# Performance work log

Hardware: AMD Instinct MI355X
Metric: run time of the kernel (lower is better)

Reference implementation:

```python
import jax, jax.numpy as jnp
import numpy as np

NV, NG, D, K, NB = 4096, 2048, 64, 128, 4
C_IN, C_OUT, E = 128, 8, 32768
SIGMA = 2.5  # rbf sigma used in the non-mp path


def _gcn_conv(x, src, dst, w, b, n):
    # PyG GCNConv (edge_weight=None, self loops already appended to src/dst)
    deg = jax.ops.segment_sum(jnp.ones(src.shape, x.dtype), dst, num_segments=n)
    dinv = jnp.where(deg > 0, 1.0 / jnp.sqrt(deg), 0.0)
    norm = dinv[src] * dinv[dst]
    h = x @ w
    return jax.ops.segment_sum(h[src] * norm[:, None], dst, num_segments=n) + b


def _diff_block(x, mass, evals, evecs, gradX, gradY, t, a_re, a_im, w0, b0, w1, b1, w2, b2):
    # learned-time spectral diffusion
    x_spec = evecs.T @ (x * mass[:, None])                      # [K, D]
    coef = jnp.exp(-evals[:, None] * jnp.clip(t, 1e-8)[None, :])  # [K, D]
    x_diff = evecs @ (coef * x_spec)                            # [NV, D]
    # spatial gradient features: complex grad, learned rotation, tanh of inner product
    gX = gradX @ x_diff                                         # real part  [NV, D]
    gY = gradY @ x_diff                                         # imag part  [NV, D]
    b_re = gX @ a_re - gY @ a_im
    b_im = gY @ a_re + gX @ a_im
    gfeat = jnp.tanh(gX * b_re + gY * b_im)
    f = jnp.concatenate([x, x_diff, gfeat], axis=-1)            # [NV, 3D]
    h = jax.nn.relu(f @ w0 + b0)
    h = jax.nn.relu(h @ w1 + b1)
    return h @ w2 + b2 + x                                      # residual skip


def _forward(surf_x, mass, evals, evecs, gradX, gradY, vertices, graph_x, graph_pos,
             lin1_w, lin1_b, lin2_w, lin2_b, last_w, last_b,
             diff_time, A_re, A_im, mlp_w0, mlp_b0, mlp_w1, mlp_b1, mlp_w2, mlp_b2,
             gcn_w1, gcn_b1, gcn_w2, gcn_b2, edge_index):
    nv, ng = vertices.shape[0], graph_pos.shape[0]
    # dense rbf coupling (torch.no_grad in original -> stop_gradient)
    d2 = (jnp.sum(vertices * vertices, 1)[:, None]
          + jnp.sum(graph_pos * graph_pos, 1)[None, :]
          - 2.0 * (vertices @ graph_pos.T))
    dist = jnp.sqrt(jnp.clip(d2, 0.0))
    rbf = jax.lax.stop_gradient(jnp.exp(-dist / SIGMA))          # [NV, NG]
    diff_x = surf_x @ lin1_w + lin1_b                            # [NV, D]
    gx = graph_x @ lin2_w + lin2_b                               # [NG, D]
    loops = jnp.arange(ng, dtype=edge_index.dtype)
    src = jnp.concatenate([edge_index[0], loops])
    dst = jnp.concatenate([edge_index[1], loops])
    for i in range(NB):
        diff_x = _diff_block(diff_x, mass, evals, evecs, gradX, gradY,
                             diff_time[i], A_re[i], A_im[i],
                             mlp_w0[i], mlp_b0[i], mlp_w1[i], mlp_b1[i], mlp_w2[i], mlp_b2[i])
        gx = rbf.T @ diff_x                                      # surface -> graph
        h = jax.nn.relu(_gcn_conv(gx, src, dst, gcn_w1[i], gcn_b1[i], ng))
        gx = _gcn_conv(h, src, dst, gcn_w2[i], gcn_b2[i], ng)
        diff_x = rbf @ gx                                        # graph -> surface
    return diff_x @ last_w + last_b                              # [NV, C_OUT]


def setup_inputs() -> dict:
    key = jax.random.key(0)
    ks = jax.random.split(key, 24)
    f32 = jnp.float32
    def rn(k, shape, scale=1.0):
        return jax.random.normal(k, shape, f32) * scale
    inp = {
        'surf_x': rn(ks[0], (NV, 5)),
        'mass': jax.random.uniform(ks[1], (NV,), f32, 0.1, 1.0),
        'evals': jnp.sort(jax.random.uniform(ks[2], (K,), f32, 0.0, 50.0)),
        'evecs': rn(ks[3], (NV, K), 1.0 / np.sqrt(NV)),
        'gradX': rn(ks[4], (NV, NV), 1.0 / np.sqrt(NV)),
        'gradY': rn(ks[5], (NV, NV), 1.0 / np.sqrt(NV)),
        'vertices': rn(ks[6], (NV, 3), 5.0),
        'graph_x': rn(ks[7], (NG, C_IN)),
        'graph_pos': rn(ks[8], (NG, 3), 5.0),
        'lin1_w': rn(ks[9], (5, D), 1.0 / np.sqrt(5)),
        'lin1_b': jnp.zeros((D,), f32),
        'lin2_w': rn(ks[10], (C_IN, D), 1.0 / np.sqrt(C_IN)),
        'lin2_b': jnp.zeros((D,), f32),
        'last_w': rn(ks[11], (D, C_OUT), 1.0 / np.sqrt(D)),
        'last_b': jnp.zeros((C_OUT,), f32),
        'diff_time': jax.random.uniform(ks[12], (NB, D), f32, 1e-3, 1.0),
        'A_re': rn(ks[13], (NB, D, D), 1.0 / np.sqrt(D)),
        'A_im': rn(ks[14], (NB, D, D), 1.0 / np.sqrt(D)),
        'mlp_w0': rn(ks[15], (NB, 3 * D, D), 1.0 / np.sqrt(3 * D)),
        'mlp_b0': jnp.zeros((NB, D), f32),
        'mlp_w1': rn(ks[16], (NB, D, D), 1.0 / np.sqrt(D)),
        'mlp_b1': jnp.zeros((NB, D), f32),
        'mlp_w2': rn(ks[17], (NB, D, D), 1.0 / np.sqrt(D)),
        'mlp_b2': jnp.zeros((NB, D), f32),
        'gcn_w1': rn(ks[18], (NB, D, D), 1.0 / np.sqrt(D)),
        'gcn_b1': jnp.zeros((NB, D), f32),
        'gcn_w2': rn(ks[19], (NB, D, D), 1.0 / np.sqrt(D)),
        'gcn_b2': jnp.zeros((NB, D), f32),
        'edge_index': jax.random.randint(ks[20], (2, E), 0, NG, dtype=jnp.int32),
    }
    return inp


def reference(surf_x, mass, evals, evecs, gradX, gradY, vertices, graph_x, graph_pos,
              lin1_w, lin1_b, lin2_w, lin2_b, last_w, last_b,
              diff_time, A_re, A_im, mlp_w0, mlp_b0, mlp_w1, mlp_b1, mlp_w2, mlp_b2,
              gcn_w1, gcn_b1, gcn_w2, gcn_b2, edge_index):
    return _forward(surf_x, mass, evals, evecs, gradX, gradY, vertices, graph_x, graph_pos,
                    lin1_w, lin1_b, lin2_w, lin2_b, last_w, last_b,
                    diff_time, A_re, A_im, mlp_w0, mlp_b0, mlp_w1, mlp_b1, mlp_w2, mlp_b2,
                    gcn_w1, gcn_b1, gcn_w2, gcn_b2, edge_index)
```

## Files before the change

### kernel.cpp

```cpp
#include <hip/hip_runtime.h>
#include <hip/hip_bf16.h>

#define NVV 4096
#define NGG 2048
#define DD 64
#define KSP 128
#define NBLK 4
#define NEDGE 32768
#define COUT 8
#define NSLICE_P 8
#define NSLICE_G 16
#define NSLICE_V 8
#define NSLICE_S 32
#define VS 32

typedef __hip_bfloat16 bf16;
using bf16x8 = __attribute__((ext_vector_type(8))) __bf16;
using s16x8  = __attribute__((ext_vector_type(8))) short;
using f32x4  = __attribute__((ext_vector_type(4))) float;

__device__ __forceinline__ float toF(bf16 x){ return __bfloat162float(x); }
__device__ __forceinline__ float ldin(const void* p, size_t i, int f){
  return f ? toF(((const bf16*)p)[i]) : ((const float*)p)[i];
}
__device__ __forceinline__ short f2bf(float x){
  __bf16 b = (__bf16)x;
  return __builtin_bit_cast(short, b);
}
__device__ __forceinline__ float bf2f(short s){
  return (float)__builtin_bit_cast(__bf16, s);
}
__device__ __forceinline__ bf16x8 ld8(const short* p){
  return __builtin_bit_cast(bf16x8, *(const s16x8*)p);
}
__device__ __forceinline__ void gl16(const short* g, short* l){
  __builtin_amdgcn_global_load_lds((__attribute__((address_space(1))) void*)(g),
                                   (__attribute__((address_space(3))) void*)(l),
                                   16, 0, 0);
}

__global__ void k_probe(const void* __restrict__ mass, int* __restrict__ flag){
  int t = threadIdx.x;
  float v = toF(((const bf16*)mass)[t]);
  bool ok = (v >= 0.05f) && (v <= 1.05f);
  unsigned long long m = __ballot(ok);
  if (t == 0) flag[0] = (m == ~0ull) ? 1 : 0;
}

__global__ void k_csr_zero(int* c){ int g = blockIdx.x*256+threadIdx.x; if (g<NGG) c[g]=0; }
__global__ void k_csr_cnt(const int* __restrict__ ei, int* __restrict__ c){
  int e = blockIdx.x*256+threadIdx.x; if (e<NEDGE) atomicAdd(&c[ei[NEDGE+e]], 1);
}
__global__ void k_csr_scan(const int* __restrict__ cnt, int* __restrict__ off,
                           int* __restrict__ cursor, float* __restrict__ dinv){
  __shared__ int ws[256];
  int t = threadIdx.x;
  int base = t*8;
  int local[8]; int s = 0;
  #pragma unroll
  for (int i=0;i<8;i++){ local[i]=s; s += cnt[base+i]; }
  ws[t] = s;
  __syncthreads();
  for (int o=1;o<256;o<<=1){
    int v = (t>=o) ? ws[t-o] : 0;
    __syncthreads();
    ws[t] += v;
    __syncthreads();
  }
  int pre = (t==0) ? 0 : ws[t-1];
  #pragma unroll
  for (int i=0;i<8;i++){
    int o = pre + local[i];
    off[base+i] = o; cursor[base+i] = o;
    dinv[base+i] = rsqrtf(1.f + (float)cnt[base+i]);
  }
  if (t==255) off[NGG] = pre + s;
}
__global__ void k_csr_fill(const int* __restrict__ ei, int* __restrict__ cursor,
                           int* __restrict__ csrc){
  int e = blockIdx.x*256+threadIdx.x;
  if (e < NEDGE){
    int d = ei[NEDGE+e];
    int p = atomicAdd(&cursor[d], 1);
    csrc[p] = ei[e];
  }
}

__global__ void k_lin1_mx(const void* __restrict__ sx, const void* __restrict__ w,
                          const void* __restrict__ b, const void* __restrict__ mass,
                          float* __restrict__ out, short* __restrict__ btMX,
                          const int* __restrict__ flg){
  const int f = *flg;
  __shared__ short tl[64*68];
  const int t = threadIdx.x;
  const int r = t>>2, c0 = (t&3)*16;
  const size_t v = (size_t)blockIdx.x*64 + r;
  float sxa[5];
  #pragma unroll
  for (int k=0;k<5;k++) sxa[k] = ldin(sx, v*5+k, f);
  const float mv = ldin(mass, v, f);
  float acc[16];
  #pragma unroll
  for (int j=0;j<16;j++){
    float a = ldin(b, c0+j, f);
    #pragma unroll
    for (int k=0;k<5;k++) a += sxa[k]*ldin(w, (size_t)k*DD + c0 + j, f);
    acc[j] = a;
    tl[(size_t)(c0+j)*68 + r] = f2bf(a*mv);
  }
  float* op = out + v*DD + c0;
  ((float4*)op)[0] = *(float4*)&acc[0];
  ((float4*)op)[1] = *(float4*)&acc[4];
  ((float4*)op)[2] = *(float4*)&acc[8];
  ((float4*)op)[3] = *(float4*)&acc[12];
  __syncthreads();
  s16x8 u0, u1;
  #pragma unroll
  for (int j=0;j<8;j++){ u0[j]=tl[(size_t)r*68+c0+j]; u1[j]=tl[(size_t)r*68+c0+8+j]; }
  const int s8 = (r&7)<<3;
  short* dp = btMX + (size_t)blockIdx.x*4096 + (size_t)r*64;
  *(s16x8*)&dp[c0 ^ s8]     = u0;
  *(s16x8*)&dp[(c0+8) ^ s8] = u1;
}

__global__ void k_spec_red(const float* __restrict__ partial, const void* __restrict__ evals,
                           const void* __restrict__ tvec, int boff,
                           short* __restrict__ btA, const int* __restrict__ flg){
  const int f = *flg;
  int idx = blockIdx.x*256 + threadIdx.x;
  int k = idx >> 6, d = idx & 63;
  float sum = 0.f;
  #pragma unroll 8
  for (int s = 0; s < VS; s++) sum += partial[(size_t)s*KSP*DD + idx];
  float t = fmaxf(ldin(tvec, boff + d, f), 1e-8f);
  float val = expf(-ldin(evals, k, f) * t) * sum;
  btA[(size_t)(k>>6)*4096 + (size_t)d*64 + ((k&63) ^ ((d&7)<<3))] = f2bf(val);
}

__global__ void k_cvt_a(const void* __restrict__ src, short* __restrict__ dst,
                        int Kfull, const int* __restrict__ flg){
  const int f = *flg;
  const int t = threadIdx.x;
  const int r = t>>2, c0 = (t&3)*16;
  const size_t row = (size_t)blockIdx.x*64 + r;
  const size_t base = row*(size_t)Kfull + (size_t)blockIdx.y*64 + c0;
  s16x8 v0, v1;
  if (f){
    const short* sp = (const short*)src + base;
    v0 = ((const s16x8*)sp)[0];
    v1 = ((const s16x8*)sp)[1];
  } else {
    const float* sp = (const float*)src + base;
    float tmp[16];
    ((float4*)tmp)[0] = ((const float4*)sp)[0];
    ((float4*)tmp)[1] = ((const float4*)sp)[1];
    ((float4*)tmp)[2] = ((const float4*)sp)[2];
    ((float4*)tmp)[3] = ((const float4*)sp)[3];
    #pragma unroll
    for (int i=0;i<8;i++){ v0[i]=f2bf(tmp[i]); v1[i]=f2bf(tmp[8+i]); }
  }
  const int s8 = (r&7)<<3;
  short* dp = dst + ((size_t)blockIdx.x*(Kfull>>6) + blockIdx.y)*4096 + (size_t)r*64;
  *(s16x8*)&dp[c0 ^ s8]     = v0;
  *(s16x8*)&dp[(c0+8) ^ s8] = v1;
}

__global__ void k_cvt_at(const void* __restrict__ evecs, short* __restrict__ dst,
                         const int* __restrict__ flg){
  const int f = *flg;
  __shared__ short tl[64*68];
  const int t = threadIdx.x;
  const int r = t>>2, c0 = (t&3)*16;
  const int kt = blockIdx.x, s = blockIdx.y;
  const size_t v = (size_t)kt*64 + r;
  #pragma unroll
  for (int j=0;j<16;j++)
    tl[(size_t)(c0+j)*68 + r] = f2bf(ldin(evecs, v*KSP + (size_t)s*64 + c0 + j, f));
  __syncthreads();
  s16x8 u0, u1;
  #pragma unroll
  for (int j=0;j<8;j++){ u0[j]=tl[(size_t)r*68+c0+j]; u1[j]=tl[(size_t)r*68+c0+8+j]; }
  const int s8 = (r&7)<<3;
  short* dp = dst + ((size_t)s*64 + kt)*4096 + (size_t)r*64;
  *(s16x8*)&dp[c0 ^ s8]     = u0;
  *(s16x8*)&dp[(c0+8) ^ s8] = u1;
}

__global__ void k_rbf_pre(const void* __restrict__ P, const void* __restrict__ Q,
                          short* __restrict__ rbfV, short* __restrict__ rbfG,
                          const int* __restrict__ flg){
  const int f = *flg;
  __shared__ short tl[64*68];
  const int t = threadIdx.x;
  const int r = t>>2, c0 = (t&3)*16;
  const int vt = blockIdx.x, gt = blockIdx.y;
  const float px = ldin(P, ((size_t)vt*64+r)*3+0, f);
  const float py = ldin(P, ((size_t)vt*64+r)*3+1, f);
  const float pz = ldin(P, ((size_t)vt*64+r)*3+2, f);
  s16x8 v0, v1;
  #pragma unroll
  for (int j=0;j<16;j++){
    const size_t g = (size_t)gt*64 + c0 + j;
    float dx = px - ldin(Q, g*3+0, f);
    float dy = py - ldin(Q, g*3+1, f);
    float dz = pz - ldin(Q, g*3+2, f);
    short s = f2bf(__expf(-sqrtf(dx*dx+dy*dy+dz*dz)*0.4f));
    if (j<8) v0[j] = s; else v1[j-8] = s;
    tl[(size_t)(c0+j)*68 + r] = s;
  }
  const int s8 = (r&7)<<3;
  short* vp = rbfV + ((size_t)vt*(NGG/64) + gt)*4096 + (size_t)r*64;
  *(s16x8*)&vp[c0 ^ s8]     = v0;
  *(s16x8*)&vp[(c0+8) ^ s8] = v1;
  __syncthreads();
  s16x8 u0, u1;
  #pragma unroll
  for (int j=0;j<8;j++){ u0[j] = tl[(size_t)r*68 + c0 + j]; u1[j] = tl[(size_t)r*68 + c0 + 8 + j]; }
  short* gp = rbfG + ((size_t)gt*(NVV/64) + vt)*4096 + (size_t)r*64;
  *(s16x8*)&gp[c0 ^ s8]     = u0;
  *(s16x8*)&gp[(c0+8) ^ s8] = u1;
}

__global__ void k_cvt_wt(const void* __restrict__ Are, const void* __restrict__ Aim,
                         const void* __restrict__ w0, const void* __restrict__ w1,
                         const void* __restrict__ w2,
                         short* __restrict__ btRe, short* __restrict__ btIm,
                         short* __restrict__ btW0, short* __restrict__ btW1,
                         short* __restrict__ btW2, const int* __restrict__ flg){
  const int f = *flg;
  __shared__ short tl[64*68];
  const int t = threadIdx.x;
  const int r = t>>2, c0 = (t&3)*16;
  const int slot = blockIdx.x, b = blockIdx.y;
  const void* src; size_t soff; short* dst; float scale = 1.f;
  switch(slot){
    case 0: src=Are; soff=(size_t)b*4096; dst=btRe + (size_t)b*2*4096;               break;
    case 1: src=Aim; soff=(size_t)b*4096; dst=btRe + (size_t)b*2*4096 + 4096; scale=-1.f; break;
    case 2: src=Aim; soff=(size_t)b*4096; dst=btIm + (size_t)b*2*4096;               break;
    case 3: src=Are; soff=(size_t)b*4096; dst=btIm + (size_t)b*2*4096 + 4096;        break;
    case 4: case 5: case 6:
      src=w0; soff=(size_t)b*3*4096 + (size_t)(slot-4)*4096;
      dst=btW0 + (size_t)b*3*4096 + (size_t)(slot-4)*4096;                           break;
    case 7: src=w1; soff=(size_t)b*4096; dst=btW1 + (size_t)b*4096;                  break;
    default: src=w2; soff=(size_t)b*4096; dst=btW2 + (size_t)b*4096;                 break;
  }
  #pragma unroll
  for (int j=0;j<16;j++)
    tl[(size_t)(c0+j)*68 + r] = f2bf(scale * ldin(src, soff + (size_t)r*64 + c0 + j, f));
  __syncthreads();
  s16x8 u0, u1;
  #pragma unroll
  for (int j=0;j<8;j++){ u0[j]=tl[(size_t)r*68+c0+j]; u1[j]=tl[(size_t)r*68+c0+8+j]; }
  const int s8 = (r&7)<<3;
  short* dp = dst + (size_t)r*64;
  *(s16x8*)&dp[c0 ^ s8]     = u0;
  *(s16x8*)&dp[(c0+8) ^ s8] = u1;
}

template<int TWO>
__global__ void k_gemm_pre(const short* __restrict__ A0, const short* __restrict__ A1,
                           const short* __restrict__ Bt, float* __restrict__ C,
                           int M, int ktt, int tps, int yoff, short* __restrict__ btOut){
  constexpr int NBUF = TWO ? 3 : 2;
  __shared__ __align__(16) short sm[2*NBUF*4096];
  const int t = threadIdx.x;
  const int w = t>>6, lane = t&63;
  const int fr = lane&15, fq = lane>>4;
  const int strip = blockIdx.x, sl = blockIdx.y;
  const size_t abase = ((size_t)strip*ktt + (size_t)sl*tps)*4096;
  const short* gA0 = A0 + abase;
  const short* gA1 = TWO ? (A1 + abase) : A0;
  const short* gB  = Bt + (size_t)sl*tps*4096;
  const int to = t*8;

  auto stage = [&](int p, int kt){
    short* l = &sm[p*NBUF*4096];
    const size_t ko = (size_t)kt*4096;
    gl16(gA0 + ko + to,        l + (w<<9));
    gl16(gA0 + ko + 2048 + to, l + 2048 + (w<<9));
    if (TWO){
      gl16(gA1 + ko + to,        l + 4096 + (w<<9));
      gl16(gA1 + ko + 2048 + to, l + 6144 + (w<<9));
    }
    short* lb = l + (TWO ? 8192 : 4096);
    gl16(gB + ko + to,        lb + (w<<9));
    gl16(gB + ko + 2048 + to, lb + 2048 + (w<<9));
  };

  f32x4 acc0[4] = {{0,0,0,0},{0,0,0,0},{0,0,0,0},{0,0,0,0}};
  f32x4 acc1[4] = {{0,0,0,0},{0,0,0,0},{0,0,0,0},{0,0,0,0}};

  stage(0, 0);
  int cur = 0;
  const int arow = w*16 + fr;
  const int ax0 = arow*64;
  const int asw = (arow&7)<<3;
  for (int kt=0; kt<tps; ++kt){
    if (kt+1 < tps){
      stage(cur^1, kt+1);
      if constexpr (TWO) asm volatile("s_waitcnt vmcnt(6)" ::: "memory");
      else               asm volatile("s_waitcnt vmcnt(4)" ::: "memory");
    } else {
      asm volatile("s_waitcnt vmcnt(0)" ::: "memory");
    }
    __builtin_amdgcn_s_barrier();
    asm volatile("" ::: "memory");
    const short* As  = &sm[cur*NBUF*4096];
    const short* A1s = As + 4096;
    const short* Bs  = As + (TWO ? 8192 : 4096);
    #pragma unroll
    for (int ks=0; ks<2; ks++){
      const int kx = ks*32 + fq*8;
      bf16x8 a0 = ld8(&As[ax0 + (kx ^ asw)]);
      bf16x8 a1 = TWO ? ld8(&A1s[ax0 + (kx ^ asw)]) : a0;
      #pragma unroll
      for (int nc=0;nc<4;nc++){
        const int brow = nc*16 + fr;
        bf16x8 b = ld8(&Bs[brow*64 + (kx ^ ((brow&7)<<3))]);
        acc0[nc] = __builtin_amdgcn_mfma_f32_16x16x32_bf16(a0, b, acc0[nc], 0, 0, 0);
        if constexpr (TWO)
          acc1[nc] = __builtin_amdgcn_mfma_f32_16x16x32_bf16(a1, b, acc1[nc], 0, 0, 0);
      }
    }
    asm volatile("" ::: "memory");
    __builtin_amdgcn_s_barrier();
    cur ^= 1;
  }
  float* C0 = C + (size_t)sl*M*DD;
  const int row0 = strip*64 + w*16 + fq*4;
  #pragma unroll
  for (int nc=0;nc<4;nc++)
    #pragma unroll
    for (int r=0;r<4;r++)
      C0[(size_t)(row0+r)*DD + nc*16 + fr] = acc0[nc][r];
  if constexpr (TWO){
    float* C1 = C + (size_t)yoff + (size_t)sl*M*DD;
    #pragma unroll
    for (int nc=0;nc<4;nc++)
      #pragma unroll
      for (int r=0;r<4;r++)
        C1[(size_t)(row0+r)*DD + nc*16 + fr] = acc1[nc][r];
  }
  if (btOut){
    #pragma unroll
    for (int nc=0;nc<4;nc++)
      #pragma unroll
      for (int r=0;r<4;r++){
        int k = row0 + r, n = nc*16 + fr;
        btOut[(size_t)(k>>6)*4096 + (size_t)n*64 + ((k&63) ^ ((n&7)<<3))] = f2bf(acc0[nc][r]);
      }
  }
}

__global__ void k_fold_at(const float* __restrict__ part, short* __restrict__ dX,
                          short* __restrict__ dY, int s){
  const int t = threadIdx.x;
  const int r = t>>2, c0 = (t&3)*16;
  const int strip = blockIdx.x;
  float ax[16], ay[16];
  #pragma unroll
  for (int j=0;j<16;j++){ ax[j]=0.f; ay[j]=0.f; }
  const float* pb = part + ((size_t)strip*64 + r)*DD + c0;
  for (int sl=0; sl<NSLICE_P; sl++){
    const float* px = pb + (size_t)sl*NVV*DD;
    const float* py = pb + (size_t)(sl+NSLICE_P)*NVV*DD;
    #pragma unroll
    for (int q=0;q<4;q++){
      float4 a = ((const float4*)px)[q];
      float4 b = ((const float4*)py)[q];
      ax[q*4+0]+=a.x; ax[q*4+1]+=a.y; ax[q*4+2]+=a.z; ax[q*4+3]+=a.w;
      ay[q*4+0]+=b.x; ay[q*4+1]+=b.y; ay[q*4+2]+=b.z; ay[q*4+3]+=b.w;
    }
  }
  s16x8 x0,x1,y0,y1;
  #pragma unroll
  for (int j=0;j<8;j++){ x0[j]=f2bf(ax[j]); x1[j]=f2bf(ax[8+j]);
                         y0[j]=f2bf(ay[j]); y1[j]=f2bf(ay[8+j]); }
  const int s8 = (r&7)<<3;
  short* dpx = dX + ((size_t)strip*2 + s)*4096 + (size_t)r*64;
  short* dpy = dY + ((size_t)strip*2 + s)*4096 + (size_t)r*64;
  *(s16x8*)&dpx[c0 ^ s8]     = x0;
  *(s16x8*)&dpx[(c0+8) ^ s8] = x1;
  *(s16x8*)&dpy[c0 ^ s8]     = y0;
  *(s16x8*)&dpy[(c0+8) ^ s8] = y1;
}

__global__ void k_reduce_mx(const float* __restrict__ P, const void* __restrict__ mass,
                            float* __restrict__ C, short* __restrict__ btMX,
                            int slices, const int* __restrict__ flg){
  const int f = *flg;
  __shared__ short tl[64*68];
  const int t = threadIdx.x;
  const int r = t>>2, c0 = (t&3)*16;
  const size_t v = (size_t)blockIdx.x*64 + r;
  float acc[16];
  #pragma unroll
  for (int j=0;j<16;j++) acc[j] = 0.f;
  const float* pb = P + v*DD + c0;
  for (int s=0;s<slices;s++){
    const float* ps = pb + (size_t)s*NVV*DD;
    #pragma unroll
    for (int q=0;q<4;q++){
      float4 a = ((const float4*)ps)[q];
      acc[q*4+0]+=a.x; acc[q*4+1]+=a.y; acc[q*4+2]+=a.z; acc[q*4+3]+=a.w;
    }
  }
  float* op = C + v*DD + c0;
  ((float4*)op)[0] = *(float4*)&acc[0];
  ((float4*)op)[1] = *(float4*)&acc[4];
  ((float4*)op)[2] = *(float4*)&acc[8];
  ((float4*)op)[3] = *(float4*)&acc[12];
  const float mv = ldin(mass, v, f);
  #pragma unroll
  for (int j=0;j<16;j++) tl[(size_t)(c0+j)*68 + r] = f2bf(acc[j]*mv);
  __syncthreads();
  s16x8 u0, u1;
  #pragma unroll
  for (int j=0;j<8;j++){ u0[j]=tl[(size_t)r*68+c0+j]; u1[j]=tl[(size_t)r*68+c0+8+j]; }
  const int s8 = (r&7)<<3;
  short* dp = btMX + (size_t)blockIdx.x*4096 + (size_t)r*64;
  *(s16x8*)&dp[c0 ^ s8]     = u0;
  *(s16x8*)&dp[(c0+8) ^ s8] = u1;
}

__global__ void k_tail_fused(const float* __restrict__ gXp, const float* __restrict__ gYp,
                             const float* __restrict__ cur, const float* __restrict__ xdiff,
                             const short* __restrict__ btRe, const short* __restrict__ btIm,
                             const short* __restrict__ btW0, const short* __restrict__ btW1,
                             const short* __restrict__ btW2,
                             const void* __restrict__ b0, const void* __restrict__ b1,
                             const void* __restrict__ b2, int boff,
                             short* __restrict__ btOut, const int* __restrict__ flg){
  __shared__ __align__(16) short sm[8*4096];
  const int f = *flg;
  const int t = threadIdx.x;
  const int w = t>>6, lane = t&63;
  const int fr = lane&15, fq = lane>>4;
  const int strip = blockIdx.x;
  const int to = t*8;
  gl16(btRe + to,        &sm[2*4096] + (w<<9));
  gl16(btRe + 2048 + to, &sm[2*4096] + 2048 + (w<<9));
  gl16(btRe + 4096 + to, &sm[3*4096] + (w<<9));
  gl16(btRe + 6144 + to, &sm[3*4096] + 2048 + (w<<9));
  gl16(btIm + to,        &sm[4*4096] + (w<<9));
  gl16(btIm + 2048 + to, &sm[4*4096] + 2048 + (w<<9));
  gl16(btIm + 4096 + to, &sm[5*4096] + (w<<9));
  gl16(btIm + 6144 + to, &sm[5*4096] + 2048 + (w<<9));
  {
    const int r = t>>2, c0 = (t&3)*16;
    const size_t rowb = ((size_t)strip*64 + r)*DD + c0;
    float gxa[16], gya[16];
    ((float4*)gxa)[0]=((const float4*)(gXp+rowb))[0];
    ((float4*)gxa)[1]=((const float4*)(gXp+rowb))[1];
    ((float4*)gxa)[2]=((const float4*)(gXp+rowb))[2];
    ((float4*)gxa)[3]=((const float4*)(gXp+rowb))[3];
    ((float4*)gya)[0]=((const float4*)(gYp+rowb))[0];
    ((float4*)gya)[1]=((const float4*)(gYp+rowb))[1];
    ((float4*)gya)[2]=((const float4*)(gYp+rowb))[2];
    ((float4*)gya)[3]=((const float4*)(gYp+rowb))[3];
    s16x8 x0,x1,y0,y1;
    #pragma unroll
    for (int j=0;j<8;j++){ x0[j]=f2bf(gxa[j]); x1[j]=f2bf(gxa[8+j]);
                           y0[j]=f2bf(gya[j]); y1[j]=f2bf(gya[8+j]); }
    const int s8 = (r&7)<<3;
    *(s16x8*)&sm[0*4096 + r*64 + (c0 ^ s8)]     = x0;
    *(s16x8*)&sm[0*4096 + r*64 + ((c0+8) ^ s8)] = x1;
    *(s16x8*)&sm[1*4096 + r*64 + (c0 ^ s8)]     = y0;
    *(s16x8*)&sm[1*4096 + r*64 + ((c0+8) ^ s8)] = y1;
    const float* cp = cur   + ((size_t)strip*64 + r)*DD + c0;
    const float* xp = xdiff + ((size_t)strip*64 + r)*DD + c0;
    float ca[16], xa[16];
    ((float4*)ca)[0]=((const float4*)cp)[0]; ((float4*)ca)[1]=((const float4*)cp)[1];
    ((float4*)ca)[2]=((const float4*)cp)[2]; ((float4*)ca)[3]=((const float4*)cp)[3];
    ((float4*)xa)[0]=((const float4*)xp)[0]; ((float4*)xa)[1]=((const float4*)xp)[1];
    ((float4*)xa)[2]=((const float4*)xp)[2]; ((float4*)xa)[3]=((const float4*)xp)[3];
    s16x8 v0,v1,u0,u1;
    #pragma unroll
    for (int j=0;j<8;j++){ v0[j]=f2bf(ca[j]); v1[j]=f2bf(ca[8+j]);
                           u0[j]=f2bf(xa[j]); u1[j]=f2bf(xa[8+j]); }
    *(s16x8*)&sm[6*4096 + r*64 + (c0 ^ s8)]     = v0;
    *(s16x8*)&sm[6*4096 + r*64 + ((c0+8) ^ s8)] = v1;
    *(s16x8*)&sm[7*4096 + r*64 + (c0 ^ s8)]     = u0;
    *(s16x8*)&sm[7*4096 + r*64 + ((c0+8) ^ s8)] = u1;
  }
  __syncthreads();
  const int arow = w*16 + fr;
  const int asw = (arow&7)<<3;
  f32x4 re[4] = {{0,0,0,0},{0,0,0,0},{0,0,0,0},{0,0,0,0}};
  f32x4 im[4] = {{0,0,0,0},{0,0,0,0},{0,0,0,0},{0,0,0,0}};
  #pragma unroll
  for (int kt=0; kt<2; kt++){
    const short* As = &sm[kt*4096];
    const short* Br = &sm[(2+kt)*4096];
    const short* Bi = &sm[(4+kt)*4096];
    #pragma unroll
    for (int ks=0; ks<2; ks++){
      const int kx = ks*32 + fq*8;
      bf16x8 a = ld8(&As[arow*64 + (kx ^ asw)]);
      #pragma unroll
      for (int nc=0;nc<4;nc++){
        const int brow = nc*16 + fr, bsw = (brow&7)<<3;
        bf16x8 br_ = ld8(&Br[brow*64 + (kx ^ bsw)]);
        bf16x8 bi_ = ld8(&Bi[brow*64 + (kx ^ bsw)]);
        re[nc] = __builtin_amdgcn_mfma_f32_16x16x32_bf16(a, br_, re[nc], 0, 0, 0);
        im[nc] = __builtin_amdgcn_mfma_f32_16x16x32_bf16(a, bi_, im[nc], 0, 0, 0);
      }
    }
  }
  __syncthreads();
  gl16(btW0 + to,           &sm[2*4096] + (w<<9));
  gl16(btW0 + 2048 + to,    &sm[2*4096] + 2048 + (w<<9));
  gl16(btW0 + 4096 + to,    &sm[3*4096] + (w<<9));
  gl16(btW0 + 6144 + to,    &sm[3*4096] + 2048 + (w<<9));
  gl16(btW0 + 8192 + to,    &sm[4*4096] + (w<<9));
  gl16(btW0 + 10240 + to,   &sm[4*4096] + 2048 + (w<<9));
  gl16(btW1 + to,           &sm[5*4096] + (w<<9));
  gl16(btW1 + 2048 + to,    &sm[5*4096] + 2048 + (w<<9));
  float gfv[4][4];
  #pragma unroll
  for (int nc=0;nc<4;nc++){
    const int n = nc*16 + fr;
    #pragma unroll
    for (int r2=0;r2<4;r2++){
      const int mi = w*16 + fq*4 + r2;
      const int pos = mi*64 + (n ^ ((mi&7)<<3));
      float gx = bf2f(sm[pos]);
      float gy = bf2f(sm[4096 + pos]);
      gfv[nc][r2] = tanhf(gx*re[nc][r2] + gy*im[nc][r2]);
    }
  }
  __syncthreads();
  gl16(btW2 + to,        &sm[1*4096] + (w<<9));
  gl16(btW2 + 2048 + to, &sm[1*4096] + 2048 + (w<<9));
  #pragma unroll
  for (int nc=0;nc<4;nc++)
    #pragma unroll
    for (int r2=0;r2<4;r2++){
      const int mi = w*16 + fq*4 + r2, n = nc*16 + fr;
      sm[mi*64 + (n ^ ((mi&7)<<3))] = f2bf(gfv[nc][r2]);
    }
  __syncthreads();
  f32x4 acc[4] = {{0,0,0,0},{0,0,0,0},{0,0,0,0},{0,0,0,0}};
  #pragma unroll
  for (int kt=0; kt<3; kt++){
    const short* As = &sm[(kt==0 ? 6 : (kt==1 ? 7 : 0))*4096];
    const short* Bs = &sm[(2+kt)*4096];
    #pragma unroll
    for (int ks=0; ks<2; ks++){
      const int kx = ks*32 + fq*8;
      bf16x8 a = ld8(&As[arow*64 + (kx ^ asw)]);
      #pragma unroll
      for (int nc=0;nc<4;nc++){
        const int brow = nc*16 + fr;
        bf16x8 b = ld8(&Bs[brow*64 + (kx ^ ((brow&7)<<3))]);
        acc[nc] = __builtin_amdgcn_mfma_f32_16x16x32_bf16(a, b, acc[nc], 0, 0, 0);
      }
    }
  }
  __syncthreads();
  #pragma unroll
  for (int nc=0;nc<4;nc++){
    float bz = ldin(b0, boff + nc*16 + fr, f);
    #pragma unroll
    for (int r2=0;r2<4;r2++){
      const int mi = w*16 + fq*4 + r2, n = nc*16 + fr;
      sm[6*4096 + mi*64 + (n ^ ((mi&7)<<3))] = f2bf(fmaxf(acc[nc][r2] + bz, 0.f));
    }
  }
  __syncthreads();
  f32x4 a1c[4] = {{0,0,0,0},{0,0,0,0},{0,0,0,0},{0,0,0,0}};
  #pragma unroll
  for (int ks=0; ks<2; ks++){
    const int kx = ks*32 + fq*8;
    bf16x8 a = ld8(&sm[6*4096 + arow*64 + (kx ^ asw)]);
    #pragma unroll
    for (int nc=0;nc<4;nc++){
      const int brow = nc*16 + fr;
      bf16x8 b = ld8(&sm[5*4096 + brow*64 + (kx ^ ((brow&7)<<3))]);
      a1c[nc] = __builtin_amdgcn_mfma_f32_16x16x32_bf16(a, b, a1c[nc], 0, 0, 0);
    }
  }
  #pragma unroll
  for (int nc=0;nc<4;nc++){
    float bz = ldin(b1, boff + nc*16 + fr, f);
    #pragma unroll
    for (int r2=0;r2<4;r2++){
      const int mi = w*16 + fq*4 + r2, n = nc*16 + fr;
      sm[7*4096 + mi*64 + (n ^ ((mi&7)<<3))] = f2bf(fmaxf(a1c[nc][r2] + bz, 0.f));
    }
  }
  __syncthreads();
  f32x4 a2c[4] = {{0,0,0,0},{0,0,0,0},{0,0,0,0},{0,0,0,0}};
  #pragma unroll
  for (int ks=0; ks<2; ks++){
    const int kx = ks*32 + fq*8;
    bf16x8 a = ld8(&sm[7*4096 + arow*64 + (kx ^ asw)]);
    #pragma unroll
    for (int nc=0;nc<4;nc++){
      const int brow = nc*16 + fr;
      bf16x8 b = ld8(&sm[1*4096 + brow*64 + (kx ^ ((brow&7)<<3))]);
      a2c[nc] = __builtin_amdgcn_mfma_f32_16x16x32_bf16(a, b, a2c[nc], 0, 0, 0);
    }
  }
  const int row0 = strip*64 + w*16 + fq*4;
  #pragma unroll
  for (int nc=0;nc<4;nc++){
    float bz = ldin(b2, boff + nc*16 + fr, f);
    #pragma unroll
    for (int r2=0;r2<4;r2++){
      int row = row0 + r2, n = nc*16 + fr;
      float vv = a2c[nc][r2] + bz + cur[(size_t)row*DD + n];
      btOut[(size_t)(row>>6)*4096 + (size_t)n*64 + ((row&63) ^ ((n&7)<<3))] = f2bf(vv);
    }
  }
}

__global__ void k_gcn1(const float* __restrict__ part, const void* __restrict__ W,
                       int woff, const float* __restrict__ dinv,
                       const void* __restrict__ bias, int boff,
                       float* __restrict__ tmp, float* __restrict__ outinit,
                       const int* __restrict__ flg){
  const int f = *flg;
  __shared__ float xs[4][DD];
  int d = threadIdx.x & 63, vl = threadIdx.x >> 6;
  size_t g = (size_t)blockIdx.x*4 + vl;
  float x = 0.f;
  #pragma unroll
  for (int s = 0; s < NSLICE_G; s++) x += part[(size_t)s*NGG*DD + g*DD + d];
  xs[vl][d] = x;
  __syncthreads();
  float acc = 0.f;
  #pragma unroll 8
  for (int k=0;k<DD;k++) acc += xs[vl][k]*ldin(W, (size_t)woff + k*DD + d, f);
  tmp[g*DD+d] = acc;
  float di = dinv[g];
  outinit[g*DD+d] = acc*di*di + ldin(bias, boff + d, f);
}

__global__ void k_gcn2f(const float* __restrict__ selfinit, const float* __restrict__ tmp,
                        const int* __restrict__ off, const int* __restrict__ csrc,
                        const float* __restrict__ dinv, const void* __restrict__ W,
                        int woff, const void* __restrict__ bias, int boff,
                        float* __restrict__ tmp2, float* __restrict__ out2init,
                        const int* __restrict__ flg){
  const int f = *flg;
  __shared__ float xs[4][DD];
  int d = threadIdx.x & 63, vl = threadIdx.x >> 6;
  size_t g = (size_t)blockIdx.x*4 + vl;
  float dg = dinv[g];
  float agg = selfinit[g*DD+d];
  int s1 = off[g+1];
  for (int i = off[g]; i < s1; i++){
    int sv = csrc[i];
    agg += tmp[(size_t)sv*DD+d]*(dinv[sv]*dg);
  }
  xs[vl][d] = fmaxf(agg, 0.f);
  __syncthreads();
  float acc = 0.f;
  #pragma unroll 8
  for (int k=0;k<DD;k++) acc += xs[vl][k]*ldin(W, (size_t)woff + k*DD + d, f);
  tmp2[g*DD+d] = acc;
  out2init[g*DD+d] = acc*dg*dg + ldin(bias, boff + d, f);
}

__global__ void k_aggr_t(const float* __restrict__ selfinit, const float* __restrict__ tmp,
                         const int* __restrict__ off, const int* __restrict__ csrc,
                         const float* __restrict__ dinv, short* __restrict__ dst){
  __shared__ short tl[64*68];
  const int t = threadIdx.x;
  const int r = t>>2, c0 = (t&3)*16;
  const size_t g = (size_t)blockIdx.x*64 + r;
  const float dg = dinv[g];
  float agg[16];
  const float* sp = selfinit + g*DD + c0;
  ((float4*)agg)[0] = ((const float4*)sp)[0];
  ((float4*)agg)[1] = ((const float4*)sp)[1];
  ((float4*)agg)[2] = ((const float4*)sp)[2];
  ((float4*)agg)[3] = ((const float4*)sp)[3];
  const int e1 = off[g+1];
  for (int i = off[g]; i < e1; i++){
    const int sv = csrc[i];
    const float w_ = dinv[sv]*dg;
    const float* tp = tmp + (size_t)sv*DD + c0;
    #pragma unroll
    for (int q=0;q<4;q++){
      float4 a = ((const float4*)tp)[q];
      agg[q*4+0]+=a.x*w_; agg[q*4+1]+=a.y*w_; agg[q*4+2]+=a.z*w_; agg[q*4+3]+=a.w*w_;
    }
  }
  #pragma unroll
  for (int j=0;j<16;j++) tl[(size_t)(c0+j)*68 + r] = f2bf(agg[j]);
  __syncthreads();
  s16x8 u0,u1;
  #pragma unroll
  for (int j=0;j<8;j++){ u0[j]=tl[(size_t)r*68+c0+j]; u1[j]=tl[(size_t)r*68+c0+8+j]; }
  const int s8 = (r&7)<<3;
  short* dp = dst + (size_t)blockIdx.x*4096 + (size_t)r*64;
  *(s16x8*)&dp[c0 ^ s8]     = u0;
  *(s16x8*)&dp[(c0+8) ^ s8] = u1;
}

__global__ void k_final(const float* __restrict__ x, const void* __restrict__ w,
                        const void* __restrict__ b, void* __restrict__ outv,
                        const int* __restrict__ flg){
  const int f = *flg;
  int idx = blockIdx.x*256 + threadIdx.x;
  int v = idx >> 3, c = idx & 7;
  float acc = ldin(b, c, f);
  #pragma unroll 8
  for (int k=0;k<DD;k++) acc += x[(size_t)v*DD+k]*ldin(w, (size_t)k*COUT+c, f);
  if (f) ((bf16*)outv)[idx] = __float2bfloat16(acc);
  else   ((float*)outv)[idx] = acc;
}

extern "C" void kernel_launch(void* const* d_in, const int* in_sizes, int n_in,
                              void* d_out, int out_size, void* d_ws, size_t ws_size,
                              hipStream_t stream){
  (void)in_sizes; (void)n_in;
  const void* surf_x   = d_in[0];
  const void* mass     = d_in[1];
  const void* evals    = d_in[2];
  const void* evecs    = d_in[3];
  const void* gradX    = d_in[4];
  const void* gradY    = d_in[5];
  const void* vertices = d_in[6];
  const void* gpos     = d_in[8];
  const void* lin1_w   = d_in[9];
  const void* lin1_b   = d_in[10];
  const void* last_w   = d_in[13];
  const void* last_b   = d_in[14];
  const void* dtime    = d_in[15];
  const void* A_re     = d_in[16];
  const void* A_im     = d_in[17];
  const void* mw0      = d_in[18];
  const void* mb0      = d_in[19];
  const void* mw1      = d_in[20];
  const void* mb1      = d_in[21];
  const void* mw2      = d_in[22];
  const void* mb2      = d_in[23];
  const void* gw1      = d_in[24];
  const void* gb1      = d_in[25];
  const void* gw2      = d_in[26];
  const void* gb2      = d_in[27];
  const int*  ei       = (const int*)d_in[28];

  const size_t REQUIRED = (size_t)126*1024*1024;
  if (ws_size < REQUIRED){
    hipMemsetAsync(d_out, 0, (size_t)out_size*2, stream);
    return;
  }
  char* p = (char*)d_ws;
  auto alloc = [&](size_t bytes)->void*{
    void* r = (void*)p;
    p += (bytes + 255) & ~(size_t)255;
    return r;
  };
  float* part  = (float*)alloc((size_t)16*NVV*DD*4);
  float* bufA  = (float*)alloc((size_t)NVV*DD*4);
  float* xdiff = (float*)alloc((size_t)NVV*DD*4);
  float* tmpg  = (float*)alloc((size_t)NGG*DD*4);
  float* hg    = (float*)alloc((size_t)NGG*DD*4);
  float* tmp2  = (float*)alloc((size_t)NGG*DD*4);
  float* o2    = (float*)alloc((size_t)NGG*DD*4);
  float* dinv  = (float*)alloc((size_t)NGG*4);
  int*   flg   = (int*)alloc(256);
  int*   cnt   = (int*)alloc((size_t)NGG*4);
  int*   off   = (int*)alloc((size_t)(NGG+1)*4);
  int*   curs  = (int*)alloc((size_t)NGG*4);
  int*   csrc  = (int*)alloc((size_t)NEDGE*4);
  short* gXs   = (short*)alloc((size_t)NVV*NVV*2);
  short* gYs   = (short*)alloc((size_t)NVV*NVV*2);
  short* rbfV  = (short*)alloc((size_t)NVV*NGG*2);
  short* rbfG  = (short*)alloc((size_t)NVV*NGG*2);
  short* evsT  = (short*)alloc((size_t)NVV*KSP*2);
  short* evs   = (short*)alloc((size_t)NVV*KSP*2);
  short* GXE   = (short*)alloc((size_t)NVV*KSP*2);
  short* GYE   = (short*)alloc((size_t)NVV*KSP*2);
  short* btA   = (short*)alloc((size_t)KSP*DD*2);
  short* btB   = (short*)alloc((size_t)NVV*DD*2);
  short* btMX  = (short*)alloc((size_t)NVV*DD*2);
  short* btRe  = (short*)alloc((size_t)NBLK*2*4096*2);
  short* btIm  = (short*)alloc((size_t)NBLK*2*4096*2);
  short* btW0  = (short*)alloc((size_t)NBLK*3*4096*2);
  short* btW1  = (short*)alloc((size_t)NBLK*4096*2);
  short* btW2  = (short*)alloc((size_t)NBLK*4096*2);

  k_probe<<<1, 64, 0, stream>>>(mass, flg);
  k_csr_zero<<<NGG/256, 256, 0, stream>>>(cnt);
  k_csr_cnt <<<NEDGE/256, 256, 0, stream>>>(ei, cnt);
  k_csr_scan<<<1, 256, 0, stream>>>(cnt, off, curs, dinv);
  k_csr_fill<<<NEDGE/256, 256, 0, stream>>>(ei, curs, csrc);
  k_lin1_mx <<<NVV/64, 256, 0, stream>>>(surf_x, lin1_w, lin1_b, mass, bufA, btMX, flg);
  k_cvt_a<<<dim3(NVV/64, NVV/64), 256, 0, stream>>>(gradX, gXs, NVV, flg);
  k_cvt_a<<<dim3(NVV/64, NVV/64), 256, 0, stream>>>(gradY, gYs, NVV, flg);
  k_cvt_a<<<dim3(NVV/64, KSP/64), 256, 0, stream>>>(evecs, evs, KSP, flg);
  k_cvt_at<<<dim3(NVV/64, KSP/64), 256, 0, stream>>>(evecs, evsT, flg);
  k_rbf_pre<<<dim3(NVV/64, NGG/64), 256, 0, stream>>>(vertices, gpos, rbfV, rbfG, flg);
  k_cvt_wt<<<dim3(9, NBLK), 256, 0, stream>>>(A_re, A_im, mw0, mw1, mw2,
                                              btRe, btIm, btW0, btW1, btW2, flg);
  for (int s = 0; s < 2; s++){
    k_gemm_pre<1><<<dim3(NVV/64, NSLICE_P), 256, 0, stream>>>(
        gXs, gYs, evsT + (size_t)s*64*4096, part,
        NVV, NVV/64, (NVV/64)/NSLICE_P, NSLICE_P*NVV*DD, nullptr);
    k_fold_at<<<NVV/64, 256, 0, stream>>>(part, GXE, GYE, s);
  }

  float* cur = bufA;
  for (int b = 0; b < NBLK; b++){
    k_gemm_pre<0><<<dim3(KSP/64, NSLICE_S), 256, 0, stream>>>(evsT, evsT, btMX, part,
        KSP, NVV/64, (NVV/64)/NSLICE_S, 0, nullptr);
    k_spec_red<<<KSP*DD/256, 256, 0, stream>>>(part, evals, dtime, b*DD, btA, flg);
    k_gemm_pre<0><<<dim3(NVV/64, 1), 256, 0, stream>>>(evs, evs, btA, xdiff,
        NVV, KSP/64, KSP/64, 0, nullptr);
    k_gemm_pre<1><<<dim3(NVV/64, 1), 256, 0, stream>>>(GXE, GYE, btA, part,
        NVV, 2, 2, NVV*DD, nullptr);
    k_tail_fused<<<NVV/64, 256, 0, stream>>>(part, part + (size_t)NVV*DD, cur, xdiff,
        btRe + (size_t)b*2*4096, btIm + (size_t)b*2*4096,
        btW0 + (size_t)b*3*4096, btW1 + (size_t)b*4096, btW2 + (size_t)b*4096,
        mb0, mb1, mb2, b*DD, btB, flg);
    k_gemm_pre<0><<<dim3(NGG/64, NSLICE_G), 256, 0, stream>>>(rbfG, rbfG, btB, part,
        NGG, NVV/64, (NVV/64)/NSLICE_G, 0, nullptr);
    k_gcn1<<<NGG/4, 256, 0, stream>>>(part, gw1, b*DD*DD, dinv, gb1, b*DD, tmpg, hg, flg);
    k_gcn2f<<<NGG/4, 256, 0, stream>>>(hg, tmpg, off, csrc, dinv, gw2, b*DD*DD,
                                       gb2, b*DD, tmp2, o2, flg);
    k_aggr_t<<<NGG/64, 256, 0, stream>>>(o2, tmp2, off, csrc, dinv, btB);
    k_gemm_pre<0><<<dim3(NVV/64, NSLICE_V), 256, 0, stream>>>(rbfV, rbfV, btB, part,
        NVV, NGG/64, (NGG/64)/NSLICE_V, 0, nullptr);
    k_reduce_mx<<<NVV/64, 256, 0, stream>>>(part, mass, cur, btMX, NSLICE_V, flg);
  }
  k_final<<<NVV*COUT/256, 256, 0, stream>>>(cur, last_w, last_b, d_out, flg);
}
```

Before: 641.1 us.

## Fuse x_diff and gradient GEMMs into the tail kernel via MFMA prologue

The two per-block launches that computed x_diff (evecs @ spectral coeffs) and the gradient projections (GXE/GYE @ coeffs) are removed. k_tail_fused now loads the evecs, GXE and GYE tiles plus the coefficient matrix into shared memory, computes all three 64x64 products with MFMA, and writes the results as bf16 straight into the LDS slots the later stages read. This saves two launches per block and the fp32 round-trip of x_diff, gX and gY through global memory, at the cost of more work, registers and LDS traffic inside one kernel. The x_diff buffer is no longer allocated.

```diff
diff --git a/kernel.cpp b/kernel.cpp
--- a/kernel.cpp
+++ b/kernel.cpp
@@ -423,8 +423,9 @@
   *(s16x8*)&dp[(c0+8) ^ s8] = u1;
 }
 
-__global__ void k_tail_fused(const float* __restrict__ gXp, const float* __restrict__ gYp,
-                             const float* __restrict__ cur, const float* __restrict__ xdiff,
+__global__ void k_tail_fused(const short* __restrict__ evsA, const short* __restrict__ GXE,
+                             const short* __restrict__ GYE, const short* __restrict__ btA,
+                             const float* __restrict__ cur,
                              const short* __restrict__ btRe, const short* __restrict__ btIm,
                              const short* __restrict__ btW0, const short* __restrict__ btW1,
                              const short* __restrict__ btW2,
@@ -438,6 +439,47 @@
   const int fr = lane&15, fq = lane>>4;
   const int strip = blockIdx.x;
   const int to = t*8;
+  const int arow = w*16 + fr;
+  const int asw = (arow&7)<<3;
+  #pragma unroll
+  for (int kt=0; kt<2; kt++){
+    const size_t ko = ((size_t)strip*2 + kt)*4096;
+    gl16(evsA + ko + to,        &sm[kt*4096] + (w<<9));
+    gl16(evsA + ko + 2048 + to, &sm[kt*4096] + 2048 + (w<<9));
+    gl16(GXE + ko + to,         &sm[(2+kt)*4096] + (w<<9));
+    gl16(GXE + ko + 2048 + to,  &sm[(2+kt)*4096] + 2048 + (w<<9));
+    gl16(GYE + ko + to,         &sm[(4+kt)*4096] + (w<<9));
+    gl16(GYE + ko + 2048 + to,  &sm[(4+kt)*4096] + 2048 + (w<<9));
+    gl16(btA + (size_t)kt*4096 + to,        &sm[(6+kt)*4096] + (w<<9));
+    gl16(btA + (size_t)kt*4096 + 2048 + to, &sm[(6+kt)*4096] + 2048 + (w<<9));
+  }
+  __syncthreads();
+  f32x4 aX[4]  = {{0,0,0,0},{0,0,0,0},{0,0,0,0},{0,0,0,0}};
+  f32x4 aGX[4] = {{0,0,0,0},{0,0,0,0},{0,0,0,0},{0,0,0,0}};
+  f32x4 aGY[4] = {{0,0,0,0},{0,0,0,0},{0,0,0,0},{0,0,0,0}};
+  #pragma unroll
+  for (int kt=0; kt<2; kt++){
+    const short* Ae = &sm[kt*4096];
+    const short* Ax = &sm[(2+kt)*4096];
+    const short* Ay = &sm[(4+kt)*4096];
+    const short* Bs = &sm[(6+kt)*4096];
+    #pragma unroll
+    for (int ks=0; ks<2; ks++){
+      const int kx = ks*32 + fq*8;
+      bf16x8 ae = ld8(&Ae[arow*64 + (kx ^ asw)]);
+      bf16x8 ax = ld8(&Ax[arow*64 + (kx ^ asw)]);
+      bf16x8 ay = ld8(&Ay[arow*64 + (kx ^ asw)]);
+      #pragma unroll
+      for (int nc=0;nc<4;nc++){
+        const int brow = nc*16 + fr;
+        bf16x8 b = ld8(&Bs[brow*64 + (kx ^ ((brow&7)<<3))]);
+        aX[nc]  = __builtin_amdgcn_mfma_f32_16x16x32_bf16(ae, b, aX[nc], 0, 0, 0);
+        aGX[nc] = __builtin_amdgcn_mfma_f32_16x16x32_bf16(ax, b, aGX[nc], 0, 0, 0);
+        aGY[nc] = __builtin_amdgcn_mfma_f32_16x16x32_bf16(ay, b, aGY[nc], 0, 0, 0);
+      }
+    }
+  }
+  __syncthreads();
   gl16(btRe + to,        &sm[2*4096] + (w<<9));
   gl16(btRe + 2048 + to, &sm[2*4096] + 2048 + (w<<9));
   gl16(btRe + 4096 + to, &sm[3*4096] + (w<<9));
@@ -446,46 +488,30 @@
   gl16(btIm + 2048 + to, &sm[4*4096] + 2048 + (w<<9));
   gl16(btIm + 4096 + to, &sm[5*4096] + (w<<9));
   gl16(btIm + 6144 + to, &sm[5*4096] + 2048 + (w<<9));
+  #pragma unroll
+  for (int nc=0;nc<4;nc++)
+    #pragma unroll
+    for (int r2=0;r2<4;r2++){
+      const int mi = w*16 + fq*4 + r2, n = nc*16 + fr;
+      const int pos = mi*64 + (n ^ ((mi&7)<<3));
+      sm[0*4096 + pos] = f2bf(aGX[nc][r2]);
+      sm[1*4096 + pos] = f2bf(aGY[nc][r2]);
+      sm[7*4096 + pos] = f2bf(aX[nc][r2]);
+    }
   {
     const int r = t>>2, c0 = (t&3)*16;
-    const size_t rowb = ((size_t)strip*64 + r)*DD + c0;
-    float gxa[16], gya[16];
-    ((float4*)gxa)[0]=((const float4*)(gXp+rowb))[0];
-    ((float4*)gxa)[1]=((const float4*)(gXp+rowb))[1];
-    ((float4*)gxa)[2]=((const float4*)(gXp+rowb))[2];
-    ((float4*)gxa)[3]=((const float4*)(gXp+rowb))[3];
-    ((float4*)gya)[0]=((const float4*)(gYp+rowb))[0];
-    ((float4*)gya)[1]=((const float4*)(gYp+rowb))[1];
-    ((float4*)gya)[2]=((const float4*)(gYp+rowb))[2];
-    ((float4*)gya)[3]=((const float4*)(gYp+rowb))[3];
-    s16x8 x0,x1,y0,y1;
-    #pragma unroll
-    for (int j=0;j<8;j++){ x0[j]=f2bf(gxa[j]); x1[j]=f2bf(gxa[8+j]);
-                           y0[j]=f2bf(gya[j]); y1[j]=f2bf(gya[8+j]); }
-    const int s8 = (r&7)<<3;
-    *(s16x8*)&sm[0*4096 + r*64 + (c0 ^ s8)]     = x0;
-    *(s16x8*)&sm[0*4096 + r*64 + ((c0+8) ^ s8)] = x1;
-    *(s16x8*)&sm[1*4096 + r*64 + (c0 ^ s8)]     = y0;
-    *(s16x8*)&sm[1*4096 + r*64 + ((c0+8) ^ s8)] = y1;
-    const float* cp = cur   + ((size_t)strip*64 + r)*DD + c0;
-    const float* xp = xdiff + ((size_t)strip*64 + r)*DD + c0;
-    float ca[16], xa[16];
+    const float* cp = cur + ((size_t)strip*64 + r)*DD + c0;
+    float ca[16];
     ((float4*)ca)[0]=((const float4*)cp)[0]; ((float4*)ca)[1]=((const float4*)cp)[1];
     ((float4*)ca)[2]=((const float4*)cp)[2]; ((float4*)ca)[3]=((const float4*)cp)[3];
-    ((float4*)xa)[0]=((const float4*)xp)[0]; ((float4*)xa)[1]=((const float4*)xp)[1];
-    ((float4*)xa)[2]=((const float4*)xp)[2]; ((float4*)xa)[3]=((const float4*)xp)[3];
-    s16x8 v0,v1,u0,u1;
-    #pragma unroll
-    for (int j=0;j<8;j++){ v0[j]=f2bf(ca[j]); v1[j]=f2bf(ca[8+j]);
-                           u0[j]=f2bf(xa[j]); u1[j]=f2bf(xa[8+j]); }
+    s16x8 v0,v1;
+    #pragma unroll
+    for (int j=0;j<8;j++){ v0[j]=f2bf(ca[j]); v1[j]=f2bf(ca[8+j]); }
+    const int s8 = (r&7)<<3;
     *(s16x8*)&sm[6*4096 + r*64 + (c0 ^ s8)]     = v0;
     *(s16x8*)&sm[6*4096 + r*64 + ((c0+8) ^ s8)] = v1;
-    *(s16x8*)&sm[7*4096 + r*64 + (c0 ^ s8)]     = u0;
-    *(s16x8*)&sm[7*4096 + r*64 + ((c0+8) ^ s8)] = u1;
-  }
-  __syncthreads();
-  const int arow = w*16 + fr;
-  const int asw = (arow&7)<<3;
+  }
+  __syncthreads();
   f32x4 re[4] = {{0,0,0,0},{0,0,0,0},{0,0,0,0},{0,0,0,0}};
   f32x4 im[4] = {{0,0,0,0},{0,0,0,0},{0,0,0,0},{0,0,0,0}};
   #pragma unroll
@@ -757,7 +783,6 @@
   };
   float* part  = (float*)alloc((size_t)16*NVV*DD*4);
   float* bufA  = (float*)alloc((size_t)NVV*DD*4);
-  float* xdiff = (float*)alloc((size_t)NVV*DD*4);
   float* tmpg  = (float*)alloc((size_t)NGG*DD*4);
   float* hg    = (float*)alloc((size_t)NGG*DD*4);
   float* tmp2  = (float*)alloc((size_t)NGG*DD*4);
@@ -810,11 +835,7 @@
     k_gemm_pre<0><<<dim3(KSP/64, NSLICE_S), 256, 0, stream>>>(evsT, evsT, btMX, part,
         KSP, NVV/64, (NVV/64)/NSLICE_S, 0, nullptr);
     k_spec_red<<<KSP*DD/256, 256, 0, stream>>>(part, evals, dtime, b*DD, btA, flg);
-    k_gemm_pre<0><<<dim3(NVV/64, 1), 256, 0, stream>>>(evs, evs, btA, xdiff,
-        NVV, KSP/64, KSP/64, 0, nullptr);
-    k_gemm_pre<1><<<dim3(NVV/64, 1), 256, 0, stream>>>(GXE, GYE, btA, part,
-        NVV, 2, 2, NVV*DD, nullptr);
-    k_tail_fused<<<NVV/64, 256, 0, stream>>>(part, part + (size_t)NVV*DD, cur, xdiff,
+    k_tail_fused<<<NVV/64, 256, 0, stream>>>(evs, GXE, GYE, btA, cur,
         btRe + (size_t)b*2*4096, btIm + (size_t)b*2*4096,
         btW0 + (size_t)b*3*4096, btW1 + (size_t)b*4096, btW2 + (size_t)b*4096,
         mb0, mb1, mb2, b*DD, btB, flg);
```

Measured after the change: 618.8 us. 3.5% less time.
